# Optimization experiments

Measured on AMD Instinct MI355X. Metric: run time of the kernel, lower is better.

## Reference

```python
import jax, jax.numpy as jnp
import numpy as np

B, T, C = 2, 2048, 512
H = 16
HS = C // H  # 32
DF = 4 * C   # 2048
EPS = 1e-3   # keras LayerNormalization default


def setup_inputs() -> dict:
    key = jax.random.key(0)
    ks = jax.random.split(key, 16)
    s = 0.02
    return {
        "x":  jax.random.normal(ks[0], (B, T, C), jnp.float32),
        "Wq": jax.random.normal(ks[1], (H, C, HS), jnp.float32) * s,
        "bq": jnp.zeros((H, HS), jnp.float32),
        "Wk": jax.random.normal(ks[2], (H, C, HS), jnp.float32) * s,
        "bk": jnp.zeros((H, HS), jnp.float32),
        "Wv": jax.random.normal(ks[3], (H, C, HS), jnp.float32) * s,
        "bv": jnp.zeros((H, HS), jnp.float32),
        "Wo": jax.random.normal(ks[4], (C, C), jnp.float32) * s,
        "bo": jnp.zeros((C,), jnp.float32),
        "W1": jax.random.normal(ks[5], (C, DF), jnp.float32) * s,
        "b1": jnp.zeros((DF,), jnp.float32),
        "W2": jax.random.normal(ks[6], (DF, C), jnp.float32) * s,
        "b2": jnp.zeros((C,), jnp.float32),
        "g1": jnp.ones((C,), jnp.float32),
        "be1": jnp.zeros((C,), jnp.float32),
        "g2": jnp.ones((C,), jnp.float32),
        "be2": jnp.zeros((C,), jnp.float32),
    }


def _layernorm(x, g, b):
    mu = jnp.mean(x, axis=-1, keepdims=True)
    var = jnp.mean(jnp.square(x - mu), axis=-1, keepdims=True)
    return (x - mu) / jnp.sqrt(var + EPS) * g + b


def reference(x, Wq, bq, Wk, bk, Wv, bv, Wo, bo, W1, b1, W2, b2, g1, be1, g2, be2):
    Bx, Tx, Cx = x.shape
    # --- attention branch (pre-LN) ---
    h = _layernorm(x, g1, be1)
    q = jnp.einsum('btc,hcd->bhtd', h, Wq) + bq[None, :, None, :]
    k = jnp.einsum('btc,hcd->bhtd', h, Wk) + bk[None, :, None, :]
    v = jnp.einsum('btc,hcd->bhtd', h, Wv) + bv[None, :, None, :]
    # NOTE: source code never applies 1/sqrt(head_size) to scores (mask-only scaling bug)
    scores = jnp.einsum('bhtd,bhsd->bhts', q, k)           # [B,H,T,T]
    causal = jnp.tril(jnp.ones((Tx, Tx), dtype=bool))
    scores = jnp.where(causal, scores, -jnp.inf)
    att = jax.nn.softmax(scores, axis=-1)
    o = jnp.einsum('bhts,bhsd->bhtd', att, v)              # [B,H,T,HS]
    o = o.transpose(0, 2, 1, 3).reshape(Bx, Tx, Cx)        # concat heads
    x = x + o @ Wo + bo
    # --- FFN branch (pre-LN) ---
    h2 = _layernorm(x, g2, be2)
    f = jax.nn.relu(h2 @ W1 + b1) @ W2 + b2
    return x + f
```

## Files before the change

kernel.cpp:

```cpp
#include <hip/hip_runtime.h>
#include <hip/hip_bf16.h>

#define T_  2048
#define C_  512
#define H_  16
#define HS_ 32
#define DF_ 2048
#define B_  2
#define M_  4096

typedef __attribute__((ext_vector_type(8))) short short8;
typedef __attribute__((ext_vector_type(4))) short short4v;
typedef __attribute__((ext_vector_type(4))) float f32x4;
typedef __attribute__((ext_vector_type(16))) float f32x16;

__device__ inline short bf16r(float f) {
  union { float f; unsigned u; } v; v.f = f;
  return (short)((v.u + 0x7FFFu + ((v.u >> 16) & 1u)) >> 16);
}

__device__ inline f32x4 mfma16(short8 a, short8 b, f32x4 c) {
  return __builtin_amdgcn_mfma_f32_16x16x32_bf16(a, b, c, 0, 0, 0);
}
__device__ inline f32x16 mfma32(short8 a, short8 b, f32x16 c) {
  return __builtin_amdgcn_mfma_f32_32x32x16_bf16(a, b, c, 0, 0, 0);
}

__device__ inline unsigned cvtpk(float lo, float hi) {
  unsigned r;
  asm("v_cvt_pk_bf16_f32 %0, %1, %2" : "=v"(r) : "v"(lo), "v"(hi));
  return r;
}

__device__ inline void gload_lds16(const short* g, short* l) {
  __builtin_amdgcn_global_load_lds(
      (const __attribute__((address_space(1))) unsigned int*)g,
      (__attribute__((address_space(3))) unsigned int*)l, 16, 0, 0);
}

__device__ inline void ln_row(int row, const float* src, const float* g,
                              const float* be, short* dst, int lane) {
  const float* xr = src + (size_t)row * C_;
  float4 a = *(const float4*)(xr + lane * 8);
  float4 b = *(const float4*)(xr + lane * 8 + 4);
  float vals[8] = {a.x, a.y, a.z, a.w, b.x, b.y, b.z, b.w};
  float s = 0.f, ss = 0.f;
  #pragma unroll
  for (int i = 0; i < 8; ++i) { s += vals[i]; ss += vals[i] * vals[i]; }
  #pragma unroll
  for (int off = 1; off < 64; off <<= 1) {
    s += __shfl_xor(s, off);
    ss += __shfl_xor(ss, off);
  }
  float mu = s * (1.f / C_);
  float rstd = rsqrtf(ss * (1.f / C_) - mu * mu + 1e-3f);
  short8 o;
  #pragma unroll
  for (int i = 0; i < 8; ++i)
    o[i] = bf16r((vals[i] - mu) * rstd * g[lane * 8 + i] + be[lane * 8 + i]);
  *(short8*)(dst + (size_t)row * C_ + lane * 8) = o;
}

__global__ __launch_bounds__(256) void prep_kernel(
    const float* __restrict__ x, const float* __restrict__ g1, const float* __restrict__ be1,
    const float* __restrict__ Wq, const float* __restrict__ Wk, const float* __restrict__ Wv,
    const float* __restrict__ Wo, const float* __restrict__ W1, const float* __restrict__ W2,
    short* __restrict__ h1, short* __restrict__ Wqkv, short* __restrict__ Wop,
    short* __restrict__ W1p, short* __restrict__ W2p) {
  __shared__ float tile[32][33];
  int id = blockIdx.x;
  int tid = threadIdx.x;
  if (id >= 3072) {
    int w = tid >> 6, lane = tid & 63;
    ln_row((id - 3072) * 4 + w, x, g1, be1, h1, lane);
    return;
  }
  const float* src; short* dst;
  int srcN, dstK, k0, n0;
  size_t dstBase;
  if (id < 768) {
    int s = id >> 4, ct = id & 15;
    int proj = s >> 4, hh = s & 15;
    src = (proj == 0 ? Wq : (proj == 1 ? Wk : Wv)) + (size_t)hh * 512 * 32;
    srcN = 32; dstK = 512; k0 = ct * 32; n0 = 0;
    dst = Wqkv; dstBase = (size_t)(proj * 512 + hh * 32);
  } else if (id < 1024) {
    int t = id - 768;
    src = Wo; srcN = 512; dstK = 512;
    k0 = (t >> 4) * 32; n0 = (t & 15) * 32; dst = Wop; dstBase = 0;
  } else if (id < 2048) {
    int t = id - 1024;
    src = W1; srcN = 2048; dstK = 512;
    k0 = (t >> 6) * 32; n0 = (t & 63) * 32; dst = W1p; dstBase = 0;
  } else {
    int t = id - 2048;
    src = W2; srcN = 512; dstK = 2048;
    k0 = (t >> 4) * 32; n0 = (t & 15) * 32; dst = W2p; dstBase = 0;
  }
  int rr = tid >> 3, rc = (tid & 7) * 4;
  float4 v4 = *(const float4*)(src + (size_t)(k0 + rr) * srcN + n0 + rc);
  tile[rr][rc + 0] = v4.x; tile[rr][rc + 1] = v4.y;
  tile[rr][rc + 2] = v4.z; tile[rr][rc + 3] = v4.w;
  __syncthreads();
  int wn = tid >> 3, wk = (tid & 7) * 4;
  short4v o;
  o[0] = bf16r(tile[wk + 0][wn]);
  o[1] = bf16r(tile[wk + 1][wn]);
  o[2] = bf16r(tile[wk + 2][wn]);
  o[3] = bf16r(tile[wk + 3][wn]);
  *(short4v*)(dst + (dstBase + n0 + wn) * (size_t)dstK + k0 + wk) = o;
}

__global__ __launch_bounds__(256) void ln2_kernel(
    const float* __restrict__ x, const float* __restrict__ g, const float* __restrict__ be,
    short* __restrict__ out) {
  int w = threadIdx.x >> 6, lane = threadIdx.x & 63;
  ln_row(blockIdx.x * 4 + w, x, g, be, out, lane);
}

template<int BM, int BN, int WM, int WN, int KDIM, int FM, int FN>
__device__ inline void gemm_core(const short* __restrict__ A, const short* __restrict__ Bw,
                                 int m0, int n0, f32x4 (&acc)[FM][FN]) {
  static_assert(WM * WN == 4 && FM == BM / WM / 16 && FN == BN / WN / 16, "geometry");
  __shared__ short lA[2][BM * 64];
  __shared__ short lB[2][BN * 64];
  const int tid = threadIdx.x, w = tid >> 6, lane = tid & 63;
  const int cl = lane & 15, g = lane >> 4;
  const int wm = w / WN, wn = w % WN;
  const int srow = tid >> 3;
  const int sug  = (tid & 7) ^ (srow & 7);
  constexpr int NT = KDIM / 64;

  auto stage = [&](int buf, int k0) {
    #pragma unroll
    for (int j = 0; j < BM / 32; ++j)
      gload_lds16(A + (size_t)(m0 + j * 32 + srow) * KDIM + k0 + sug * 8,
                  &lA[buf][j * 2048 + tid * 8]);
    #pragma unroll
    for (int j = 0; j < BN / 32; ++j)
      gload_lds16(Bw + (size_t)(n0 + j * 32 + srow) * KDIM + k0 + sug * 8,
                  &lB[buf][j * 2048 + tid * 8]);
  };

  stage(0, 0);
  __syncthreads();
  int cur = 0;
  for (int t = 0; t < NT; ++t) {
    if (t + 1 < NT) stage(cur ^ 1, (t + 1) * 64);
    #pragma unroll
    for (int kk = 0; kk < 2; ++kk) {
      const int uswz = ((kk * 4 + g) ^ (cl & 7)) * 8;
      short8 a[FM], b[FN];
      #pragma unroll
      for (int mi = 0; mi < FM; ++mi)
        a[mi] = *(const short8*)&lA[cur][(wm * (BM / WM) + mi * 16 + cl) * 64 + uswz];
      #pragma unroll
      for (int ni = 0; ni < FN; ++ni)
        b[ni] = *(const short8*)&lB[cur][(wn * (BN / WN) + ni * 16 + cl) * 64 + uswz];
      #pragma unroll
      for (int mi = 0; mi < FM; ++mi)
        #pragma unroll
        for (int ni = 0; ni < FN; ++ni)
          acc[mi][ni] = mfma16(a[mi], b[ni], acc[mi][ni]);
    }
    __syncthreads();
    cur ^= 1;
  }
}

__global__ __launch_bounds__(256) void gemm_qkvt(
    const short* __restrict__ h1, const short* __restrict__ Wqkv,
    const float* __restrict__ bq, const float* __restrict__ bk,
    const float* __restrict__ bv,
    short* __restrict__ qb, short* __restrict__ kb, short* __restrict__ vTb) {
  int id = blockIdx.x;
  const short *Ap, *Bp;
  int m0, n0;
  bool isv = id >= 512;
  if (!isv) { m0 = (id >> 3) * 64; n0 = (id & 7) * 128; Ap = h1; Bp = Wqkv; }
  else { int t = id - 512; m0 = (t & 7) * 64; n0 = (t >> 3) * 128;
         Ap = Wqkv + 1024 * 512; Bp = h1; }
  f32x4 acc[2][4] = {};
  gemm_core<64, 128, 2, 2, 512, 2, 4>(Ap, Bp, m0, n0, acc);
  int w = threadIdx.x >> 6, lane = threadIdx.x & 63;
  int cl = lane & 15, rb = (lane >> 4) * 4;
  int wm = w >> 1, wn = w & 1;
  if (!isv) {
    #pragma unroll
    for (int mi = 0; mi < 2; ++mi)
      #pragma unroll
      for (int ni = 0; ni < 4; ++ni)
        #pragma unroll
        for (int r = 0; r < 4; ++r) {
          int mm = m0 + wm * 32 + mi * 16 + rb + r;
          int n  = n0 + wn * 64 + ni * 16 + cl;
          int proj = n >> 9, rem = n & 511;
          int hh = rem >> 5, d = rem & 31;
          int b = mm >> 11, t = mm & (T_ - 1);
          size_t bh = (size_t)b * H_ + hh;
          float val = acc[mi][ni][r];
          if (proj == 0) qb[(bh * T_ + t) * HS_ + d] = bf16r(val + bq[rem]);
          else           kb[(bh * T_ + t) * HS_ + d] = bf16r(val + bk[rem]);
        }
  } else {
    #pragma unroll
    for (int mi = 0; mi < 2; ++mi)
      #pragma unroll
      for (int ni = 0; ni < 4; ++ni)
        #pragma unroll
        for (int r = 0; r < 4; ++r) {
          int m = m0 + wm * 32 + mi * 16 + rb + r;
          int n = n0 + wn * 64 + ni * 16 + cl;
          vTb[(size_t)(n >> 11) * (512 * 2048) + (size_t)m * T_ + (n & 2047)] =
              bf16r(acc[mi][ni][r] + bv[m]);
        }
  }
}

__global__ __launch_bounds__(256) void gemm_out(
    const short* __restrict__ A, const short* __restrict__ W,
    const float* __restrict__ bo, const float* __restrict__ xres,
    float* __restrict__ x1) {
  int id = blockIdx.x;
  int xcd = id & 7, s = id >> 3;
  int m0 = (xcd * 8 + (s & 7)) * 64;
  int n0 = (s >> 3) * 64;
  f32x4 acc[2][2] = {};
  gemm_core<64, 64, 2, 2, 512, 2, 2>(A, W, m0, n0, acc);
  int w = threadIdx.x >> 6, lane = threadIdx.x & 63;
  int cl = lane & 15, rb = (lane >> 4) * 4;
  int wm = w >> 1, wn = w & 1;
  #pragma unroll
  for (int mi = 0; mi < 2; ++mi)
    #pragma unroll
    for (int ni = 0; ni < 2; ++ni)
      #pragma unroll
      for (int r = 0; r < 4; ++r) {
        int mm = m0 + wm * 32 + mi * 16 + rb + r;
        int n  = n0 + wn * 32 + ni * 16 + cl;
        x1[(size_t)mm * C_ + n] = acc[mi][ni][r] + bo[n] + xres[(size_t)mm * C_ + n];
      }
}

__global__ __launch_bounds__(256) void gemm_ffn1(
    const short* __restrict__ A, const short* __restrict__ W,
    const float* __restrict__ b1, short* __restrict__ f1) {
  int id = blockIdx.x;
  int xcd = id & 7, s = id >> 3;
  int m0 = (xcd * 4 + (s & 3)) * 128;
  int n0 = (s >> 2) * 128;
  f32x4 acc[4][4] = {};
  gemm_core<128, 128, 2, 2, 512, 4, 4>(A, W, m0, n0, acc);
  int w = threadIdx.x >> 6, lane = threadIdx.x & 63;
  int cl = lane & 15, rb = (lane >> 4) * 4;
  int wm = w >> 1, wn = w & 1;
  #pragma unroll
  for (int mi = 0; mi < 4; ++mi)
    #pragma unroll
    for (int ni = 0; ni < 4; ++ni)
      #pragma unroll
      for (int r = 0; r < 4; ++r) {
        int mm = m0 + wm * 64 + mi * 16 + rb + r;
        int n  = n0 + wn * 64 + ni * 16 + cl;
        f1[(size_t)mm * DF_ + n] = bf16r(fmaxf(acc[mi][ni][r] + b1[n], 0.f));
      }
}

__global__ __launch_bounds__(256) void gemm_ffn2(
    const short* __restrict__ A, const short* __restrict__ W,
    const float* __restrict__ b2, const float* __restrict__ x1,
    float* __restrict__ out) {
  int id = blockIdx.x;
  int xcd = id & 7, s = id >> 3;
  int m0 = (xcd * 8 + (s & 7)) * 64;
  int n0 = (s >> 3) * 64;
  f32x4 acc[2][2] = {};
  gemm_core<64, 64, 2, 2, 2048, 2, 2>(A, W, m0, n0, acc);
  int w = threadIdx.x >> 6, lane = threadIdx.x & 63;
  int cl = lane & 15, rb = (lane >> 4) * 4;
  int wm = w >> 1, wn = w & 1;
  #pragma unroll
  for (int mi = 0; mi < 2; ++mi)
    #pragma unroll
    for (int ni = 0; ni < 2; ++ni)
      #pragma unroll
      for (int r = 0; r < 4; ++r) {
        int mm = m0 + wm * 32 + mi * 16 + rb + r;
        int n  = n0 + wn * 32 + ni * 16 + cl;
        out[(size_t)mm * C_ + n] = acc[mi][ni][r] + b2[n] + x1[(size_t)mm * C_ + n];
      }
}

__global__ __launch_bounds__(256) void attn_kernel(
    const short* __restrict__ qb, const short* __restrict__ kb,
    const short* __restrict__ vTb, short* __restrict__ ob) {
  __shared__ float accbuf[4][64][17];
  __shared__ float lbuf[4][32];
  __shared__ short tbuf[32][34];
  const int id = blockIdx.x;
  const int xcd = id & 7, s = id >> 3;
  const int headin = s & 3;
  const int qt = 63 - (s >> 2);
  const int bh = xcd * 4 + headin;
  const int w = threadIdx.x >> 6, lane = threadIdx.x & 63;
  const int cl = lane & 31, g = lane >> 5;
  const int q0 = qt * 32, q = q0 + cl;
  const float L2E = 1.44269504f;
  const float NFM = -16.f * L2E;

  const short* Qp  = qb  + (size_t)bh * T_ * HS_;
  const short* Kp  = kb  + (size_t)bh * T_ * HS_;
  const short* VTp = vTb + (size_t)bh * HS_ * T_;

  const int nc   = (qt >> 1) + 1;
  const int cbeg = (nc * w) >> 2;
  const int cend = (nc * (w + 1)) >> 2;

  f32x16 acc = {};
  float l = 0.f;

  if (cbeg < cend) {
    short8 qf0 = *(const short8*)(Qp + (size_t)q * HS_ + g * 8);
    short8 qf1 = *(const short8*)(Qp + (size_t)q * HS_ + 16 + g * 8);
    const int kc0 = cbeg << 6;
    short8 k00 = *(const short8*)(Kp + (size_t)(kc0 + cl) * HS_ + g * 8);
    short8 k01 = *(const short8*)(Kp + (size_t)(kc0 + cl) * HS_ + 16 + g * 8);
    short8 k10 = *(const short8*)(Kp + (size_t)(kc0 + 32 + cl) * HS_ + g * 8);
    short8 k11 = *(const short8*)(Kp + (size_t)(kc0 + 32 + cl) * HS_ + 16 + g * 8);

    for (int c = cbeg; c < cend; ++c) {
      const int kc = c << 6;
      short8 va = *(const short8*)(VTp + (size_t)cl * T_ + kc + g * 8);
      short8 vb = *(const short8*)(VTp + (size_t)cl * T_ + kc + 16 + g * 8);
      short8 vc = *(const short8*)(VTp + (size_t)cl * T_ + kc + 32 + g * 8);
      short8 vd = *(const short8*)(VTp + (size_t)cl * T_ + kc + 48 + g * 8);

      f32x16 Z = {};
      f32x16 S0 = mfma32(k00, qf0, Z);
      S0 = mfma32(k01, qf1, S0);
      f32x16 S1 = mfma32(k10, qf0, Z);
      S1 = mfma32(k11, qf1, S1);

      if (c + 1 < cend) {
        const int kn = kc + 64;
        k00 = *(const short8*)(Kp + (size_t)(kn + cl) * HS_ + g * 8);
        k01 = *(const short8*)(Kp + (size_t)(kn + cl) * HS_ + 16 + g * 8);
        k10 = *(const short8*)(Kp + (size_t)(kn + 32 + cl) * HS_ + g * 8);
        k11 = *(const short8*)(Kp + (size_t)(kn + 32 + cl) * HS_ + 16 + g * 8);
      }

      if (c == nc - 1) {
        #pragma unroll
        for (int r = 0; r < 16; ++r) {
          int key = kc + (r & 3) + 8 * (r >> 2) + 4 * g;
          if (key > q)      S0[r] = -1e30f;
          if (key + 32 > q) S1[r] = -1e30f;
        }
      }

      float p[32];
      #pragma unroll
      for (int r = 0; r < 16; ++r) {
        p[r]      = exp2f(fmaf(S0[r], L2E, NFM));
        p[16 + r] = exp2f(fmaf(S1[r], L2E, NFM));
      }
      float sm[8];
      #pragma unroll
      for (int r = 0; r < 8; ++r)
        sm[r] = (p[r] + p[r + 8]) + (p[16 + r] + p[24 + r]);
      #pragma unroll
      for (int r = 0; r < 4; ++r) sm[r] += sm[r + 4];
      float ps = (sm[0] + sm[1]) + (sm[2] + sm[3]);
      ps += __shfl_xor(ps, 32);
      l += ps;

      #pragma unroll
      for (int sb = 0; sb < 4; ++sb) {
        unsigned L0 = cvtpk(p[sb * 8 + 0], p[sb * 8 + 1]);
        unsigned L1 = cvtpk(p[sb * 8 + 2], p[sb * 8 + 3]);
        unsigned H0 = cvtpk(p[sb * 8 + 4], p[sb * 8 + 5]);
        unsigned H1 = cvtpk(p[sb * 8 + 6], p[sb * 8 + 7]);
        auto r02 = __builtin_amdgcn_permlane32_swap(L0, H0, false, false);
        auto r13 = __builtin_amdgcn_permlane32_swap(L1, H1, false, false);
        union { unsigned u[4]; short8 v; } pb;
        pb.u[0] = r02[0]; pb.u[1] = r13[0]; pb.u[2] = r02[1]; pb.u[3] = r13[1];
        short8 vf = (sb == 0) ? va : (sb == 1) ? vb : (sb == 2) ? vc : vd;
        acc = mfma32(vf, pb.v, acc);
      }
    }
  }

  #pragma unroll
  for (int r = 0; r < 16; ++r) accbuf[w][lane][r] = acc[r];
  if (lane < 32) lbuf[w][cl] = l;
  __syncthreads();

  if (w == 0) {
    float lsum = lbuf[0][cl] + lbuf[1][cl] + lbuf[2][cl] + lbuf[3][cl];
    float inv = 1.f / lsum;
    #pragma unroll
    for (int r = 0; r < 16; ++r) {
      float v = accbuf[0][lane][r] + accbuf[1][lane][r] +
                accbuf[2][lane][r] + accbuf[3][lane][r];
      int d = (r & 3) + 8 * (r >> 2) + 4 * g;
      tbuf[cl][d] = bf16r(v * inv);
    }
  }
  __syncthreads();

  int qr = threadIdx.x >> 3, col = (threadIdx.x & 7) * 4;
  const int b = bh >> 4, hh = bh & 15;
  short4v o4;
  o4[0] = tbuf[qr][col + 0];
  o4[1] = tbuf[qr][col + 1];
  o4[2] = tbuf[qr][col + 2];
  o4[3] = tbuf[qr][col + 3];
  *(short4v*)(ob + ((size_t)b * T_ + q0 + qr) * C_ + hh * HS_ + col) = o4;
}

#define OFF_H1   ((size_t)0)
#define OFF_WQKV ((size_t)4194304)
#define OFF_WO   ((size_t)5767168)
#define OFF_W1   ((size_t)6291456)
#define OFF_W2   ((size_t)8388608)
#define OFF_Q    ((size_t)10485760)
#define OFF_K    ((size_t)14680064)
#define OFF_VT   ((size_t)18874368)
#define OFF_O    ((size_t)23068672)
#define OFF_X1   ((size_t)27262976)
#define OFF_H2   ((size_t)35651584)
#define OFF_F1   ((size_t)39845888)

extern "C" void kernel_launch(void* const* d_in, const int* in_sizes, int n_in,
                              void* d_out, int out_size, void* d_ws, size_t ws_size,
                              hipStream_t stream) {
  const float* x   = (const float*)d_in[0];
  const float* Wq  = (const float*)d_in[1];
  const float* bq  = (const float*)d_in[2];
  const float* Wk  = (const float*)d_in[3];
  const float* bk  = (const float*)d_in[4];
  const float* Wv  = (const float*)d_in[5];
  const float* bv  = (const float*)d_in[6];
  const float* Wo  = (const float*)d_in[7];
  const float* bo  = (const float*)d_in[8];
  const float* W1  = (const float*)d_in[9];
  const float* b1  = (const float*)d_in[10];
  const float* W2  = (const float*)d_in[11];
  const float* b2  = (const float*)d_in[12];
  const float* g1  = (const float*)d_in[13];
  const float* be1 = (const float*)d_in[14];
  const float* g2  = (const float*)d_in[15];
  const float* be2 = (const float*)d_in[16];

  char* ws = (char*)d_ws;
  short* h1   = (short*)(ws + OFF_H1);
  short* Wqkv = (short*)(ws + OFF_WQKV);
  short* Wop  = (short*)(ws + OFF_WO);
  short* W1p  = (short*)(ws + OFF_W1);
  short* W2p  = (short*)(ws + OFF_W2);
  short* qb   = (short*)(ws + OFF_Q);
  short* kb   = (short*)(ws + OFF_K);
  short* vTb  = (short*)(ws + OFF_VT);
  short* ob   = (short*)(ws + OFF_O);
  float* x1   = (float*)(ws + OFF_X1);
  short* h2   = (short*)(ws + OFF_H2);
  short* f1   = (short*)(ws + OFF_F1);
  float* out  = (float*)d_out;

  prep_kernel<<<3072 + 1024, 256, 0, stream>>>(x, g1, be1, Wq, Wk, Wv, Wo, W1, W2,
                                               h1, Wqkv, Wop, W1p, W2p);
  gemm_qkvt<<<768, 256, 0, stream>>>(h1, Wqkv, bq, bk, bv, qb, kb, vTb);
  attn_kernel<<<2048, 256, 0, stream>>>(qb, kb, vTb, ob);
  gemm_out<<<512, 256, 0, stream>>>(ob, Wop, bo, x, x1);
  ln2_kernel<<<M_ / 4, 256, 0, stream>>>(x1, g2, be2, h2);
  gemm_ffn1<<<512, 256, 0, stream>>>(h2, W1p, b1, f1);
  gemm_ffn2<<<512, 256, 0, stream>>>(f1, W2p, b2, x1, out);
}
```

Baseline: 107.3 us.

## Retile FFN1, double-buffer FFN2 K loop, raise MFMA priority in attention

FFN1 moves to 64x128 tiles with twice as many blocks, so more CUs stay busy. FFN2 gets its own double-buffered LDS loop with 128-wide K steps and swizzled async global-to-LDS loads, replacing the generic gemm_core to overlap loads with MFMA. The attention kernel wraps its MFMA sections in s_setprio to favour matrix issue across waves. The larger FFN2 LDS footprint (64 KB) may lower occupancy.

```diff
diff --git a/kernel.cpp b/kernel.cpp
--- a/kernel.cpp
+++ b/kernel.cpp
@@ -247,20 +247,20 @@
     const float* __restrict__ b1, short* __restrict__ f1) {
   int id = blockIdx.x;
   int xcd = id & 7, s = id >> 3;
-  int m0 = (xcd * 4 + (s & 3)) * 128;
-  int n0 = (s >> 2) * 128;
-  f32x4 acc[4][4] = {};
-  gemm_core<128, 128, 2, 2, 512, 4, 4>(A, W, m0, n0, acc);
+  int m0 = (xcd * 8 + (s & 7)) * 64;
+  int n0 = (s >> 3) * 128;
+  f32x4 acc[2][4] = {};
+  gemm_core<64, 128, 2, 2, 512, 2, 4>(A, W, m0, n0, acc);
   int w = threadIdx.x >> 6, lane = threadIdx.x & 63;
   int cl = lane & 15, rb = (lane >> 4) * 4;
   int wm = w >> 1, wn = w & 1;
   #pragma unroll
-  for (int mi = 0; mi < 4; ++mi)
+  for (int mi = 0; mi < 2; ++mi)
     #pragma unroll
     for (int ni = 0; ni < 4; ++ni)
       #pragma unroll
       for (int r = 0; r < 4; ++r) {
-        int mm = m0 + wm * 64 + mi * 16 + rb + r;
+        int mm = m0 + wm * 32 + mi * 16 + rb + r;
         int n  = n0 + wn * 64 + ni * 16 + cl;
         f1[(size_t)mm * DF_ + n] = bf16r(fmaxf(acc[mi][ni][r] + b1[n], 0.f));
       }
@@ -270,15 +270,52 @@
     const short* __restrict__ A, const short* __restrict__ W,
     const float* __restrict__ b2, const float* __restrict__ x1,
     float* __restrict__ out) {
+  __shared__ short lA[2][64 * 128];
+  __shared__ short lB[2][64 * 128];
   int id = blockIdx.x;
   int xcd = id & 7, s = id >> 3;
   int m0 = (xcd * 8 + (s & 7)) * 64;
   int n0 = (s >> 3) * 64;
+  const int tid = threadIdx.x, w = tid >> 6, lane = tid & 63;
+  const int cl = lane & 15, g = lane >> 4;
+  const int wm = w >> 1, wn = w & 1;
+  const int srow16 = tid >> 4;
+  const int sug = (tid & 15) ^ (srow16 & 7);
+  constexpr int NT = 16;
   f32x4 acc[2][2] = {};
-  gemm_core<64, 64, 2, 2, 2048, 2, 2>(A, W, m0, n0, acc);
-  int w = threadIdx.x >> 6, lane = threadIdx.x & 63;
-  int cl = lane & 15, rb = (lane >> 4) * 4;
-  int wm = w >> 1, wn = w & 1;
+
+  auto stage = [&](int buf, int k0) {
+    #pragma unroll
+    for (int j = 0; j < 4; ++j) {
+      gload_lds16(A + (size_t)(m0 + j * 16 + srow16) * DF_ + k0 + sug * 8,
+                  &lA[buf][j * 2048 + tid * 8]);
+      gload_lds16(W + (size_t)(n0 + j * 16 + srow16) * DF_ + k0 + sug * 8,
+                  &lB[buf][j * 2048 + tid * 8]);
+    }
+  };
+
+  stage(0, 0);
+  __syncthreads();
+  int cur = 0;
+  for (int t = 0; t < NT; ++t) {
+    if (t + 1 < NT) stage(cur ^ 1, (t + 1) * 128);
+    #pragma unroll
+    for (int kk = 0; kk < 4; ++kk) {
+      const int uswz = ((kk * 4 + g) ^ (cl & 7)) * 8;
+      short8 a0 = *(const short8*)&lA[cur][(wm * 32 + cl) * 128 + uswz];
+      short8 a1 = *(const short8*)&lA[cur][(wm * 32 + 16 + cl) * 128 + uswz];
+      short8 b0 = *(const short8*)&lB[cur][(wn * 32 + cl) * 128 + uswz];
+      short8 b1 = *(const short8*)&lB[cur][(wn * 32 + 16 + cl) * 128 + uswz];
+      acc[0][0] = mfma16(a0, b0, acc[0][0]);
+      acc[0][1] = mfma16(a0, b1, acc[0][1]);
+      acc[1][0] = mfma16(a1, b0, acc[1][0]);
+      acc[1][1] = mfma16(a1, b1, acc[1][1]);
+    }
+    __syncthreads();
+    cur ^= 1;
+  }
+
+  int rb = (lane >> 4) * 4;
   #pragma unroll
   for (int mi = 0; mi < 2; ++mi)
     #pragma unroll
@@ -335,11 +372,13 @@
       short8 vc = *(const short8*)(VTp + (size_t)cl * T_ + kc + 32 + g * 8);
       short8 vd = *(const short8*)(VTp + (size_t)cl * T_ + kc + 48 + g * 8);
 
+      __builtin_amdgcn_s_setprio(1);
       f32x16 Z = {};
       f32x16 S0 = mfma32(k00, qf0, Z);
       S0 = mfma32(k01, qf1, S0);
       f32x16 S1 = mfma32(k10, qf0, Z);
       S1 = mfma32(k11, qf1, S1);
+      __builtin_amdgcn_s_setprio(0);
 
       if (c + 1 < cend) {
         const int kn = kc + 64;
@@ -374,6 +413,7 @@
       ps += __shfl_xor(ps, 32);
       l += ps;
 
+      __builtin_amdgcn_s_setprio(1);
       #pragma unroll
       for (int sb = 0; sb < 4; ++sb) {
         unsigned L0 = cvtpk(p[sb * 8 + 0], p[sb * 8 + 1]);
@@ -387,6 +427,7 @@
         short8 vf = (sb == 0) ? va : (sb == 1) ? vb : (sb == 2) ? vc : vd;
         acc = mfma32(vf, pb.v, acc);
       }
+      __builtin_amdgcn_s_setprio(0);
     }
   }
 
@@ -473,6 +514,6 @@
   attn_kernel<<<2048, 256, 0, stream>>>(qb, kb, vTb, ob);
   gemm_out<<<512, 256, 0, stream>>>(ob, Wop, bo, x, x1);
   ln2_kernel<<<M_ / 4, 256, 0, stream>>>(x1, g2, be2, h2);
-  gemm_ffn1<<<512, 256, 0, stream>>>(h2, W1p, b1, f1);
+  gemm_ffn1<<<1024, 256, 0, stream>>>(h2, W1p, b1, f1);
   gemm_ffn2<<<512, 256, 0, stream>>>(f1, W2p, b2, x1, out);
 }
```

Result: faster. 103.2 us (-3.8%).
